# Kernel optimization log

Hardware: AMD Instinct MI355X
Metric: run time of the kernel (lower is better)

## Reference

```python
import jax, jax.numpy as jnp
import numpy as np


def setup_inputs() -> dict:
    key = jax.random.key(0)
    ks = jax.random.split(key, 5)
    B, in_ch, H, W = 8, 256, 128, 128
    C = in_ch // 4
    x = jax.random.normal(ks[0], (B, in_ch, H, W), dtype=jnp.float32)
    # 1x1 conv weights stored as [out_ch, in_ch] (kernel spatial dims are 1)
    w_in = jax.random.normal(ks[1], (C, in_ch), dtype=jnp.float32) * (1.0 / np.sqrt(in_ch))
    b_in = jax.random.normal(ks[2], (C,), dtype=jnp.float32) * 0.01
    w_out = jax.random.normal(ks[3], (in_ch, C), dtype=jnp.float32) * (1.0 / np.sqrt(C))
    b_out = jax.random.normal(ks[4], (in_ch,), dtype=jnp.float32) * 0.01
    detal = jnp.array([0.1], dtype=jnp.float32)
    return {"x": x, "w_in": w_in, "b_in": b_in, "w_out": w_out, "b_out": b_out, "detal": detal}


def _mda(x, w_in, b_in, w_out, b_out, detal):
    # InConv: 1x1 conv == channel GEMM
    inp = jnp.einsum('bihw,oi->bohw', x, w_in) + b_in[None, :, None, None]
    B, C, H, W = inp.shape

    # ---- W branch ----
    # AdaptiveAvgPool2d((None,1)) -> mean over W; softmax over size-1 axis (== ones, kept for faithfulness)
    f_w = jax.nn.softmax(inp.mean(axis=3, keepdims=True), axis=3)          # [B,C,H,1]
    f_w = jnp.transpose(f_w, (0, 3, 1, 2)).reshape(B, C * H, 1)
    Xw = inp.reshape(B, C * H, W)
    Gw = Xw * f_w                                                          # [B,CH,W]
    Tw = jax.nn.softmax(jnp.einsum('bkw,bkv->bwv', Gw, Gw), axis=1)        # [B,W,W], softmax over rows
    Wo = jnp.einsum('bkw,bwv->bkv', Xw, Tw).reshape(B, C, H, W)

    # ---- H branch ----
    f_h = jax.nn.softmax(jnp.transpose(inp, (0, 1, 3, 2)).mean(axis=3, keepdims=True), axis=3)  # [B,C,W,1]
    f_h = jnp.transpose(f_h, (0, 3, 1, 2)).reshape(B, C * W, 1)
    Xh = inp.reshape(B, C * W, H)  # raw .view as in torch (scrambles H/W axes intentionally)
    Gh = Xh * f_h
    Th = jax.nn.softmax(jnp.einsum('bkh,bkg->bhg', Gh, Gh), axis=1)        # [B,H,H]
    Ho = jnp.einsum('bkh,bhg->bkg', Xh, Th).reshape(B, C, H, W)

    # ---- C branch ----
    perm = jnp.transpose(inp, (0, 2, 3, 1))                                # [B,H,W,C]
    f_c = jax.nn.softmax(perm.mean(axis=3, keepdims=True), axis=3)         # [B,H,W,1]
    f_c = jnp.transpose(f_c, (0, 3, 1, 2)).reshape(B, H * W, 1)
    Xc = perm.reshape(B, H * W, C)
    Gc = f_c * Xc
    Tc = jax.nn.softmax(jnp.einsum('bnc,bnd->bcd', Gc, Gc), axis=1)        # [B,C,C]
    # torch does .view(B,C,H,W) on a [B,H*W,C] tensor: raw reshape, NOT a transpose
    Co = jnp.einsum('bnc,bcd->bnd', Xc, Tc).reshape(B, C, H, W)

    s = detal[0] * (Co + Wo + Ho)
    # OuConv 1x1 + residual
    return jnp.einsum('bchw,oc->bohw', s, w_out) + b_out[None, :, None, None] + x


def reference(x, w_in, b_in, w_out, b_out, detal):
    return _mda(x, w_in, b_in, w_out, b_out, detal)
```

## Files before the change

### kernel.cpp

```cpp
#include <hip/hip_runtime.h>
#include <math.h>

#define NB 8
#define IC 256
#define CC 64
#define HH 128
#define WW 128
#define NN (HH*WW)
#define NKW 64
#define NKC 64

static constexpr size_t SZ_INP  = (size_t)NB * CC * NN;
static constexpr size_t OFF_INP = 0;
static constexpr size_t OFF_S   = OFF_INP + SZ_INP;
static constexpr size_t OFF_PC  = OFF_S + SZ_INP;
static constexpr size_t OFF_TW  = OFF_PC + (size_t)NB * NKC * 4096;
static constexpr size_t OFF_TC  = OFF_TW + (size_t)NB * 16384;
static constexpr size_t OFF_WT  = OFF_TC + (size_t)NB * 4096;
static constexpr size_t OFF_WOT = OFF_WT + 16384;

__global__ __launch_bounds__(256) void k_wt(
    const float* __restrict__ w_in, const float* __restrict__ w_out,
    float* __restrict__ w_in_t, float* __restrict__ w_out_t)
{
    const int idx = blockIdx.x * 256 + threadIdx.x;
    if (idx < 16384) {
        const int o = idx & 63, i = idx >> 6;
        w_in_t[idx] = w_in[o * IC + i];
    } else {
        const int j = idx - 16384;
        const int o = j & 255, c = j >> 8;
        w_out_t[j] = w_out[o * CC + c];
    }
}

__global__ __launch_bounds__(256) void k_inconv(
    const float* __restrict__ x, const float* __restrict__ wt,
    const float* __restrict__ b_in, float* __restrict__ inp)
{
    __shared__ float xs[16 * 260];
    __shared__ float wl[16 * 68];
    const int b  = blockIdx.y;
    const int n0 = blockIdx.x * 256;
    const int t  = threadIdx.x;
    const int og = t >> 5;
    const int ng = t & 31;

    const int sr = t >> 4, sc = (t & 15) * 4;
    const float* xbase = x + ((size_t)b * IC + sr) * NN + n0 + sc;
    const float* wbase = wt + (size_t)sr * 64 + sc;
    float* xdst = xs + sr * 260 + sc;
    float* wdst = wl + sr * 68 + sc;

    float acc[8][8];
#pragma unroll
    for (int p = 0; p < 8; p++)
#pragma unroll
        for (int q = 0; q < 8; q++) acc[p][q] = 0.f;

    for (int i0 = 0; i0 < IC; i0 += 16) {
        __syncthreads();
        {
            const float* xsrc = xbase + (size_t)i0 * NN;
            const float4 a0 = *(const float4*)(xsrc);
            const float4 a1 = *(const float4*)(xsrc + 64);
            const float4 a2 = *(const float4*)(xsrc + 128);
            const float4 a3 = *(const float4*)(xsrc + 192);
            const float4 w0 = *(const float4*)(wbase + (size_t)i0 * 64);
            *(float4*)(xdst)       = a0;
            *(float4*)(xdst + 64)  = a1;
            *(float4*)(xdst + 128) = a2;
            *(float4*)(xdst + 192) = a3;
            *(float4*)(wdst)       = w0;
        }
        __syncthreads();
#pragma unroll 4
        for (int i = 0; i < 16; ++i) {
            const float4 wa = *(const float4*)(wl + i * 68 + og * 8);
            const float4 wb = *(const float4*)(wl + i * 68 + og * 8 + 4);
            const float4 xa = *(const float4*)(xs + i * 260 + ng * 4);
            const float4 xb = *(const float4*)(xs + i * 260 + 128 + ng * 4);
            const float wv[8] = {wa.x, wa.y, wa.z, wa.w, wb.x, wb.y, wb.z, wb.w};
            const float xv[8] = {xa.x, xa.y, xa.z, xa.w, xb.x, xb.y, xb.z, xb.w};
#pragma unroll
            for (int p = 0; p < 8; p++)
#pragma unroll
                for (int q = 0; q < 8; q++) acc[p][q] += wv[p] * xv[q];
        }
    }
#pragma unroll
    for (int p = 0; p < 8; ++p) {
        const int oo = og * 8 + p;
        const float bo = b_in[oo];
        float* base = inp + ((size_t)b * CC + oo) * NN + n0;
        *(float4*)(base + ng * 4) =
            make_float4(acc[p][0] + bo, acc[p][1] + bo, acc[p][2] + bo, acc[p][3] + bo);
        *(float4*)(base + 128 + ng * 4) =
            make_float4(acc[p][4] + bo, acc[p][5] + bo, acc[p][6] + bo, acc[p][7] + bo);
    }
}

__global__ __launch_bounds__(256) void k_gramW(const float* __restrict__ inp, float* __restrict__ pW)
{
    __shared__ float xs[32 * 132];
    const int b = blockIdx.y, kc = blockIdx.x;
    const int t = threadIdx.x, tx = t & 15, ty = t >> 4;
    const float* Xb = inp + (size_t)b * CC * NN;
    const int k0 = kc * ((CC * HH) / NKW);

    float acc[8][8];
#pragma unroll
    for (int i = 0; i < 8; i++)
#pragma unroll
        for (int j = 0; j < 8; j++) acc[i][j] = 0.f;

    for (int kk = k0; kk < k0 + (CC * HH) / NKW; kk += 32) {
        __syncthreads();
        {
            const int r = t >> 3, cq = (t & 7) * 16;
            const float* src = Xb + ((size_t)kk + r) * WW + cq;
            float* dst = xs + r * 132 + cq;
#pragma unroll
            for (int j = 0; j < 4; j++)
                *(float4*)(dst + 4 * j) = *(const float4*)(src + 4 * j);
        }
        __syncthreads();
#pragma unroll 8
        for (int k = 0; k < 32; k++) {
            const float* row = xs + k * 132;
            float4 t0 = *(const float4*)(row + ty * 8);
            float4 t1 = *(const float4*)(row + ty * 8 + 4);
            float4 u0 = *(const float4*)(row + tx * 8);
            float4 u1 = *(const float4*)(row + tx * 8 + 4);
            float av[8] = {t0.x, t0.y, t0.z, t0.w, t1.x, t1.y, t1.z, t1.w};
            float bv[8] = {u0.x, u0.y, u0.z, u0.w, u1.x, u1.y, u1.z, u1.w};
#pragma unroll
            for (int i = 0; i < 8; i++)
#pragma unroll
                for (int j = 0; j < 8; j++) acc[i][j] += av[i] * bv[j];
        }
    }
    float* dst = pW + ((size_t)b * NKW + kc) * 16384;
#pragma unroll
    for (int i = 0; i < 8; i++)
#pragma unroll
        for (int j = 0; j < 8; j += 4) {
            float4 v = make_float4(acc[i][j], acc[i][j + 1], acc[i][j + 2], acc[i][j + 3]);
            *(float4*)(dst + (ty * 8 + i) * 128 + tx * 8 + j) = v;
        }
}

__global__ __launch_bounds__(256) void k_redW(const float* __restrict__ pW, float* __restrict__ Tw)
{
    const int b = blockIdx.y;
    const int idx = blockIdx.x * 256 + threadIdx.x;
    const float* p = pW + (size_t)b * NKW * 16384 + idx;
    float acc = 0.f;
#pragma unroll
    for (int k = 0; k < NKW; k++) acc += p[(size_t)k * 16384];
    Tw[(size_t)b * 16384 + idx] = acc;
}

__global__ __launch_bounds__(1024) void k_softW(float* __restrict__ Tw)
{
    __shared__ float red[32 * 33];
    const int b = blockIdx.x, v0 = blockIdx.y * 32;
    const int t = threadIdx.x;
    const int vc = t & 31, wg = t >> 5;
    float* S = Tw + (size_t)b * 16384 + v0 + vc;

    float v[4];
    float m = -3.4e38f;
#pragma unroll
    for (int j = 0; j < 4; j++) { v[j] = S[(wg * 4 + j) * 128]; m = fmaxf(m, v[j]); }
    red[wg * 33 + vc] = m;
    __syncthreads();
    for (int st = 16; st > 0; st >>= 1) {
        if (wg < st) red[wg * 33 + vc] = fmaxf(red[wg * 33 + vc], red[(wg + st) * 33 + vc]);
        __syncthreads();
    }
    m = red[vc];
    __syncthreads();
    float sum = 0.f;
#pragma unroll
    for (int j = 0; j < 4; j++) { v[j] = __expf(v[j] - m); sum += v[j]; }
    red[wg * 33 + vc] = sum;
    __syncthreads();
    for (int st = 16; st > 0; st >>= 1) {
        if (wg < st) red[wg * 33 + vc] += red[(wg + st) * 33 + vc];
        __syncthreads();
    }
    const float inv = 1.f / red[vc];
#pragma unroll
    for (int j = 0; j < 4; j++) S[(wg * 4 + j) * 128] = v[j] * inv;
}

__global__ __launch_bounds__(256) void k_gramC(const float* __restrict__ inp, float* __restrict__ pC)
{
    __shared__ float xt[32 * 68];
    const int b = blockIdx.y, nc = blockIdx.x;
    const int t = threadIdx.x, tx = t & 15, ty = t >> 4;
    const float* ip = inp + (size_t)b * CC * NN;
    const int n0 = nc * (NN / NKC);

    float acc[4][4];
#pragma unroll
    for (int i = 0; i < 4; i++)
#pragma unroll
        for (int j = 0; j < 4; j++) acc[i][j] = 0.f;

    const int scc = t >> 2;
    const int sn  = (t & 3) * 8;

    for (int nt = 0; nt < NN / NKC; nt += 32) {
        __syncthreads();
        {
            const float* src = ip + (size_t)scc * NN + n0 + nt + sn;
            float v[8];
            *(float4*)(v)     = *(const float4*)(src);
            *(float4*)(v + 4) = *(const float4*)(src + 4);
#pragma unroll
            for (int j = 0; j < 8; j++) xt[(sn + j) * 68 + scc] = v[j];
        }
        __syncthreads();
#pragma unroll 8
        for (int nn = 0; nn < 32; nn++) {
            const float4 a4 = *(const float4*)(xt + nn * 68 + ty * 4);
            const float4 e4 = *(const float4*)(xt + nn * 68 + tx * 4);
            const float av[4] = {a4.x, a4.y, a4.z, a4.w};
            const float ev[4] = {e4.x, e4.y, e4.z, e4.w};
#pragma unroll
            for (int i = 0; i < 4; i++)
#pragma unroll
                for (int j = 0; j < 4; j++) acc[i][j] += av[i] * ev[j];
        }
    }
    float* dst = pC + ((size_t)b * NKC + nc) * 4096;
#pragma unroll
    for (int i = 0; i < 4; i++) {
        float4 v = make_float4(acc[i][0], acc[i][1], acc[i][2], acc[i][3]);
        *(float4*)(dst + (ty * 4 + i) * 64 + tx * 4) = v;
    }
}

__global__ __launch_bounds__(256) void k_redC(const float* __restrict__ pC, float* __restrict__ Tc)
{
    const int b = blockIdx.y;
    const int idx = blockIdx.x * 256 + threadIdx.x;
    const float* p = pC + (size_t)b * NKC * 4096 + idx;
    float acc = 0.f;
#pragma unroll
    for (int k = 0; k < NKC; k++) acc += p[(size_t)k * 4096];
    Tc[(size_t)b * 4096 + idx] = acc;
}

__global__ __launch_bounds__(1024) void k_softC(float* __restrict__ Tc)
{
    __shared__ float red[16 * 65];
    const int b = blockIdx.x;
    const int t = threadIdx.x;
    const int dc = t & 63, cg = t >> 6;
    float* S = Tc + (size_t)b * 4096 + dc;

    float v[4];
    float m = -3.4e38f;
#pragma unroll
    for (int j = 0; j < 4; j++) { v[j] = S[(cg * 4 + j) * 64]; m = fmaxf(m, v[j]); }
    red[cg * 65 + dc] = m;
    __syncthreads();
    for (int st = 8; st > 0; st >>= 1) {
        if (cg < st) red[cg * 65 + dc] = fmaxf(red[cg * 65 + dc], red[(cg + st) * 65 + dc]);
        __syncthreads();
    }
    m = red[dc];
    __syncthreads();
    float sum = 0.f;
#pragma unroll
    for (int j = 0; j < 4; j++) { v[j] = __expf(v[j] - m); sum += v[j]; }
    red[cg * 65 + dc] = sum;
    __syncthreads();
    for (int st = 8; st > 0; st >>= 1) {
        if (cg < st) red[cg * 65 + dc] += red[(cg + st) * 65 + dc];
        __syncthreads();
    }
    const float inv = 1.f / red[dc];
#pragma unroll
    for (int j = 0; j < 4; j++) S[(cg * 4 + j) * 64] = v[j] * inv;
}

__global__ __launch_bounds__(256) void k_co(
    const float* __restrict__ inp, const float* __restrict__ Tc,
    const float* __restrict__ detal, float* __restrict__ s)
{
    __shared__ float tc[64 * 68];
    __shared__ float xs[64 * 132];
    const int b  = blockIdx.y;
    const int n0 = blockIdx.x * 128;
    const int t  = threadIdx.x;
    const int d4 = (t & 15) * 4;
    const int g8 = (t >> 4) * 8;

    {
        const int sr = t >> 2, sc = (t & 3) * 4;
        const float* src = inp + ((size_t)b * CC + sr) * NN + n0;
        float* dst = xs + sr * 132;
#pragma unroll
        for (int k = 0; k < 8; k++)
            *(float4*)(dst + sc + 16 * k) = *(const float4*)(src + sc + 16 * k);
        const float* tsrc = Tc + (size_t)b * 4096 + sr * 64;
        float* tdst = tc + sr * 68;
#pragma unroll
        for (int k = 0; k < 4; k++)
            *(float4*)(tdst + sc + 16 * k) = *(const float4*)(tsrc + sc + 16 * k);
    }
    __syncthreads();

    float acc[8][4];
#pragma unroll
    for (int i = 0; i < 8; i++)
#pragma unroll
        for (int j = 0; j < 4; j++) acc[i][j] = 0.f;

#pragma unroll 4
    for (int c = 0; c < 64; c++) {
        const float4 t4 = *(const float4*)(tc + c * 68 + d4);
        const float4 xa = *(const float4*)(xs + c * 132 + g8);
        const float4 xb = *(const float4*)(xs + c * 132 + g8 + 4);
        const float xv[8] = {xa.x, xa.y, xa.z, xa.w, xb.x, xb.y, xb.z, xb.w};
        const float tv[4] = {t4.x, t4.y, t4.z, t4.w};
#pragma unroll
        for (int i = 0; i < 8; i++)
#pragma unroll
            for (int j = 0; j < 4; j++) acc[i][j] += xv[i] * tv[j];
    }
    const float scl = detal[0];
    float* sb = s + (size_t)b * CC * NN + (size_t)n0 * 64;
#pragma unroll
    for (int i = 0; i < 8; i++) {
        float4 v = make_float4(acc[i][0] * scl, acc[i][1] * scl,
                               acc[i][2] * scl, acc[i][3] * scl);
        *(float4*)(sb + (size_t)(g8 + i) * 64 + d4) = v;
    }
}

__global__ __launch_bounds__(128) void k_wo(
    const float* __restrict__ inp, const float* __restrict__ Tw,
    const float* __restrict__ detal, float* __restrict__ s)
{
    __shared__ float xt[32 * 68];
    __shared__ float twl[32 * 132];
    const int b = blockIdx.z, hc = blockIdx.y, c = blockIdx.x;
    const int t = threadIdx.x;
    const int rg = t >> 4;
    const int vg = t & 15;
    const int h0 = hc * 64;

    const float* ip = inp + ((size_t)b * CC + c) * NN + (size_t)h0 * WW;
    const float* twg = Tw + (size_t)b * 16384;

    float acc[8][8];
#pragma unroll
    for (int p = 0; p < 8; p++)
#pragma unroll
        for (int q = 0; q < 8; q++) acc[p][q] = 0.f;

    for (int w0 = 0; w0 < 128; w0 += 32) {
        __syncthreads();
        {
            const int h = t >> 1, wq = (t & 1) * 16;
            const float* src = ip + (size_t)h * WW + w0 + wq;
            float v[16];
            *(float4*)(v)      = *(const float4*)(src);
            *(float4*)(v + 4)  = *(const float4*)(src + 4);
            *(float4*)(v + 8)  = *(const float4*)(src + 8);
            *(float4*)(v + 12) = *(const float4*)(src + 12);
#pragma unroll
            for (int j = 0; j < 16; j++) xt[(wq + j) * 68 + h] = v[j];
        }
        {
            const int w = t >> 2, cq = (t & 3) * 32;
            const float* src = twg + (size_t)(w0 + w) * 128 + cq;
            float* dst = twl + w * 132 + cq;
#pragma unroll
            for (int k = 0; k < 8; k++)
                *(float4*)(dst + 4 * k) = *(const float4*)(src + 4 * k);
        }
        __syncthreads();
#pragma unroll 4
        for (int w = 0; w < 32; ++w) {
            const float4 ra = *(const float4*)(xt + w * 68 + rg * 8);
            const float4 rb = *(const float4*)(xt + w * 68 + rg * 8 + 4);
            const float4 ta = *(const float4*)(twl + w * 132 + vg * 4);
            const float4 tb = *(const float4*)(twl + w * 132 + 64 + vg * 4);
            const float rv[8] = {ra.x, ra.y, ra.z, ra.w, rb.x, rb.y, rb.z, rb.w};
            const float tv[8] = {ta.x, ta.y, ta.z, ta.w, tb.x, tb.y, tb.z, tb.w};
#pragma unroll
            for (int p = 0; p < 8; p++)
#pragma unroll
                for (int q = 0; q < 8; q++) acc[p][q] += rv[p] * tv[q];
        }
    }

    const float sc2 = 2.0f * detal[0];
    float* sp = s + ((size_t)b * CC + c) * NN + (size_t)h0 * WW;
#pragma unroll
    for (int p = 0; p < 8; ++p) {
        const int h = rg * 8 + p;
        float* q0 = sp + (size_t)h * WW + vg * 4;
        float* q1 = sp + (size_t)h * WW + 64 + vg * 4;
        float4 c0 = *(const float4*)q0;
        float4 c1 = *(const float4*)q1;
        c0.x += sc2 * acc[p][0]; c0.y += sc2 * acc[p][1];
        c0.z += sc2 * acc[p][2]; c0.w += sc2 * acc[p][3];
        c1.x += sc2 * acc[p][4]; c1.y += sc2 * acc[p][5];
        c1.z += sc2 * acc[p][6]; c1.w += sc2 * acc[p][7];
        *(float4*)q0 = c0;
        *(float4*)q1 = c1;
    }
}

__global__ __launch_bounds__(256) void k_outconv(
    const float* __restrict__ s, const float* __restrict__ wot,
    const float* __restrict__ b_out, const float* __restrict__ x,
    float* __restrict__ outp)
{
    __shared__ float ss[16 * 68];
    __shared__ float wl[16 * 260];
    const int b  = blockIdx.y;
    const int n0 = blockIdx.x * 64;
    const int t  = threadIdx.x;
    const int og = t >> 3;
    const int ng = t & 7;

    const int sr = t >> 4;
    const int sq = (t & 15) * 4;
    const int wq = (t & 15) * 16;
    const float* sbase = s + ((size_t)b * CC + sr) * NN + n0 + sq;
    const float* wbase = wot + (size_t)sr * IC + wq;
    float* sdst = ss + sr * 68 + sq;
    float* wdst = wl + sr * 260 + wq;

    float acc[8][8];
#pragma unroll
    for (int p = 0; p < 8; p++)
#pragma unroll
        for (int q = 0; q < 8; q++) acc[p][q] = 0.f;

    for (int c0 = 0; c0 < CC; c0 += 16) {
        __syncthreads();
        {
            const float4 a0 = *(const float4*)(sbase + (size_t)c0 * NN);
            const float* wsrc = wbase + (size_t)c0 * IC;
            const float4 w0 = *(const float4*)(wsrc);
            const float4 w1 = *(const float4*)(wsrc + 4);
            const float4 w2 = *(const float4*)(wsrc + 8);
            const float4 w3 = *(const float4*)(wsrc + 12);
            *(float4*)(sdst)      = a0;
            *(float4*)(wdst)      = w0;
            *(float4*)(wdst + 4)  = w1;
            *(float4*)(wdst + 8)  = w2;
            *(float4*)(wdst + 12) = w3;
        }
        __syncthreads();
#pragma unroll 4
        for (int c = 0; c < 16; ++c) {
            const float4 wa = *(const float4*)(wl + c * 260 + og * 8);
            const float4 wb = *(const float4*)(wl + c * 260 + og * 8 + 4);
            const float4 sa = *(const float4*)(ss + c * 68 + ng * 4);
            const float4 sb = *(const float4*)(ss + c * 68 + 32 + ng * 4);
            const float wv[8] = {wa.x, wa.y, wa.z, wa.w, wb.x, wb.y, wb.z, wb.w};
            const float sv[8] = {sa.x, sa.y, sa.z, sa.w, sb.x, sb.y, sb.z, sb.w};
#pragma unroll
            for (int p = 0; p < 8; p++)
#pragma unroll
                for (int q = 0; q < 8; q++) acc[p][q] += wv[p] * sv[q];
        }
    }

#pragma unroll
    for (int p = 0; p < 8; ++p) {
        const int oo = og * 8 + p;
        const float bo = b_out[oo];
        const float* xb = x + ((size_t)b * IC + oo) * NN + n0;
        float* ob = outp + ((size_t)b * IC + oo) * NN + n0;
        const float4 x0 = *(const float4*)(xb + ng * 4);
        const float4 x1 = *(const float4*)(xb + 32 + ng * 4);
        *(float4*)(ob + ng * 4) =
            make_float4(acc[p][0] + bo + x0.x, acc[p][1] + bo + x0.y,
                        acc[p][2] + bo + x0.z, acc[p][3] + bo + x0.w);
        *(float4*)(ob + 32 + ng * 4) =
            make_float4(acc[p][4] + bo + x1.x, acc[p][5] + bo + x1.y,
                        acc[p][6] + bo + x1.z, acc[p][7] + bo + x1.w);
    }
}

extern "C" void kernel_launch(void* const* d_in, const int* in_sizes, int n_in,
                              void* d_out, int out_size, void* d_ws, size_t ws_size,
                              hipStream_t stream)
{
    const float* x     = (const float*)d_in[0];
    const float* w_in  = (const float*)d_in[1];
    const float* b_in  = (const float*)d_in[2];
    const float* w_out = (const float*)d_in[3];
    const float* b_out = (const float*)d_in[4];
    const float* detal = (const float*)d_in[5];
    float* out = (float*)d_out;

    float* ws   = (float*)d_ws;
    float* inp  = ws + OFF_INP;
    float* s    = ws + OFF_S;
    float* pW   = ws + OFF_S;
    float* pC   = ws + OFF_PC;
    float* Tw   = ws + OFF_TW;
    float* Tc   = ws + OFF_TC;
    float* wt   = ws + OFF_WT;
    float* wot  = ws + OFF_WOT;

    k_wt     <<<dim3(128),              256, 0, stream>>>(w_in, w_out, wt, wot);
    k_inconv <<<dim3(NN / 256, NB),     256, 0, stream>>>(x, wt, b_in, inp);
    k_gramW  <<<dim3(NKW, NB),          256, 0, stream>>>(inp, pW);
    k_redW   <<<dim3(64, NB),           256, 0, stream>>>(pW, Tw);
    k_softW  <<<dim3(NB, 4),           1024, 0, stream>>>(Tw);
    k_gramC  <<<dim3(NKC, NB),          256, 0, stream>>>(inp, pC);
    k_redC   <<<dim3(16, NB),           256, 0, stream>>>(pC, Tc);
    k_softC  <<<dim3(NB),              1024, 0, stream>>>(Tc);
    k_co     <<<dim3(NN / 128, NB),     256, 0, stream>>>(inp, Tc, detal, s);
    k_wo     <<<dim3(CC, 2, NB),        128, 0, stream>>>(inp, Tw, detal, s);
    k_outconv<<<dim3(NN / 64, NB),      256, 0, stream>>>(s, wot, b_out, x, out);
}
```

Before: 444.4 us.

## Use fp16 MFMA for input and output 1x1 convolutions

```diff
diff --git a/kernel.cpp b/kernel.cpp
--- a/kernel.cpp
+++ b/kernel.cpp
@@ -10,6 +10,9 @@
 #define NKW 64
 #define NKC 64
 
+typedef _Float16 f16x8 __attribute__((ext_vector_type(8)));
+typedef float f32x4 __attribute__((ext_vector_type(4)));
+
 static constexpr size_t SZ_INP  = (size_t)NB * CC * NN;
 static constexpr size_t OFF_INP = 0;
 static constexpr size_t OFF_S   = OFF_INP + SZ_INP;
@@ -21,83 +24,88 @@
 
 __global__ __launch_bounds__(256) void k_wt(
     const float* __restrict__ w_in, const float* __restrict__ w_out,
-    float* __restrict__ w_in_t, float* __restrict__ w_out_t)
+    _Float16* __restrict__ wh, _Float16* __restrict__ woh)
 {
     const int idx = blockIdx.x * 256 + threadIdx.x;
-    if (idx < 16384) {
-        const int o = idx & 63, i = idx >> 6;
-        w_in_t[idx] = w_in[o * IC + i];
-    } else {
-        const int j = idx - 16384;
-        const int o = j & 255, c = j >> 8;
-        w_out_t[j] = w_out[o * CC + c];
-    }
+    if (idx < 16384) wh[idx] = (_Float16)w_in[idx];
+    else             woh[idx - 16384] = (_Float16)w_out[idx - 16384];
 }
 
 __global__ __launch_bounds__(256) void k_inconv(
-    const float* __restrict__ x, const float* __restrict__ wt,
+    const float* __restrict__ x, const _Float16* __restrict__ wh,
     const float* __restrict__ b_in, float* __restrict__ inp)
 {
-    __shared__ float xs[16 * 260];
-    __shared__ float wl[16 * 68];
+    __shared__ _Float16 wl[64 * 264];
+    __shared__ _Float16 xh[32 * 136];
     const int b  = blockIdx.y;
-    const int n0 = blockIdx.x * 256;
+    const int n0 = blockIdx.x * 128;
     const int t  = threadIdx.x;
-    const int og = t >> 5;
-    const int ng = t & 31;
-
-    const int sr = t >> 4, sc = (t & 15) * 4;
-    const float* xbase = x + ((size_t)b * IC + sr) * NN + n0 + sc;
-    const float* wbase = wt + (size_t)sr * 64 + sc;
-    float* xdst = xs + sr * 260 + sc;
-    float* wdst = wl + sr * 68 + sc;
-
-    float acc[8][8];
-#pragma unroll
-    for (int p = 0; p < 8; p++)
-#pragma unroll
-        for (int q = 0; q < 8; q++) acc[p][q] = 0.f;
-
-    for (int i0 = 0; i0 < IC; i0 += 16) {
+    const int l  = t & 63, wv = t >> 6;
+    const int lr = l & 15, kg = (l >> 4) * 8;
+
+    {
+        const int r = t >> 2, c = (t & 3) * 64;
+        const uint4* src = (const uint4*)(wh + r * 256 + c);
+        uint4* dst = (uint4*)(wl + r * 264 + c);
+#pragma unroll
+        for (int k = 0; k < 8; k++) dst[k] = src[k];
+    }
+
+    f32x4 acc[4][2];
+#pragma unroll
+    for (int mt = 0; mt < 4; mt++)
+#pragma unroll
+        for (int nt = 0; nt < 2; nt++) acc[mt][nt] = (f32x4){0.f, 0.f, 0.f, 0.f};
+
+    for (int kc = 0; kc < 8; ++kc) {
         __syncthreads();
         {
-            const float* xsrc = xbase + (size_t)i0 * NN;
-            const float4 a0 = *(const float4*)(xsrc);
-            const float4 a1 = *(const float4*)(xsrc + 64);
-            const float4 a2 = *(const float4*)(xsrc + 128);
-            const float4 a3 = *(const float4*)(xsrc + 192);
-            const float4 w0 = *(const float4*)(wbase + (size_t)i0 * 64);
-            *(float4*)(xdst)       = a0;
-            *(float4*)(xdst + 64)  = a1;
-            *(float4*)(xdst + 128) = a2;
-            *(float4*)(xdst + 192) = a3;
-            *(float4*)(wdst)       = w0;
-        }
-        __syncthreads();
-#pragma unroll 4
-        for (int i = 0; i < 16; ++i) {
-            const float4 wa = *(const float4*)(wl + i * 68 + og * 8);
-            const float4 wb = *(const float4*)(wl + i * 68 + og * 8 + 4);
-            const float4 xa = *(const float4*)(xs + i * 260 + ng * 4);
-            const float4 xb = *(const float4*)(xs + i * 260 + 128 + ng * 4);
-            const float wv[8] = {wa.x, wa.y, wa.z, wa.w, wb.x, wb.y, wb.z, wb.w};
-            const float xv[8] = {xa.x, xa.y, xa.z, xa.w, xb.x, xb.y, xb.z, xb.w};
-#pragma unroll
-            for (int p = 0; p < 8; p++)
-#pragma unroll
-                for (int q = 0; q < 8; q++) acc[p][q] += wv[p] * xv[q];
-        }
-    }
-#pragma unroll
-    for (int p = 0; p < 8; ++p) {
-        const int oo = og * 8 + p;
-        const float bo = b_in[oo];
-        float* base = inp + ((size_t)b * CC + oo) * NN + n0;
-        *(float4*)(base + ng * 4) =
-            make_float4(acc[p][0] + bo, acc[p][1] + bo, acc[p][2] + bo, acc[p][3] + bo);
-        *(float4*)(base + 128 + ng * 4) =
-            make_float4(acc[p][4] + bo, acc[p][5] + bo, acc[p][6] + bo, acc[p][7] + bo);
-    }
+            const int i = t >> 3, nq = (t & 7) * 16;
+            const float* src = x + ((size_t)b * IC + kc * 32 + i) * NN + n0 + nq;
+            const float4 v0 = *(const float4*)(src);
+            const float4 v1 = *(const float4*)(src + 4);
+            const float4 v2 = *(const float4*)(src + 8);
+            const float4 v3 = *(const float4*)(src + 12);
+            f16x8 h0, h1;
+            h0[0] = (_Float16)v0.x; h0[1] = (_Float16)v0.y;
+            h0[2] = (_Float16)v0.z; h0[3] = (_Float16)v0.w;
+            h0[4] = (_Float16)v1.x; h0[5] = (_Float16)v1.y;
+            h0[6] = (_Float16)v1.z; h0[7] = (_Float16)v1.w;
+            h1[0] = (_Float16)v2.x; h1[1] = (_Float16)v2.y;
+            h1[2] = (_Float16)v2.z; h1[3] = (_Float16)v2.w;
+            h1[4] = (_Float16)v3.x; h1[5] = (_Float16)v3.y;
+            h1[6] = (_Float16)v3.z; h1[7] = (_Float16)v3.w;
+            *(f16x8*)(xh + i * 136 + nq)     = h0;
+            *(f16x8*)(xh + i * 136 + nq + 8) = h1;
+        }
+        __syncthreads();
+
+        f16x8 bf[2];
+#pragma unroll
+        for (int nt = 0; nt < 2; ++nt) {
+            const int n = wv * 32 + nt * 16 + lr;
+#pragma unroll
+            for (int j = 0; j < 8; ++j) bf[nt][j] = xh[(kg + j) * 136 + n];
+        }
+#pragma unroll
+        for (int mt = 0; mt < 4; ++mt) {
+            const f16x8 af = *(const f16x8*)(wl + (mt * 16 + lr) * 264 + kc * 32 + kg);
+            acc[mt][0] = __builtin_amdgcn_mfma_f32_16x16x32_f16(af, bf[0], acc[mt][0], 0, 0, 0);
+            acc[mt][1] = __builtin_amdgcn_mfma_f32_16x16x32_f16(af, bf[1], acc[mt][1], 0, 0, 0);
+        }
+    }
+
+#pragma unroll
+    for (int mt = 0; mt < 4; ++mt)
+#pragma unroll
+        for (int nt = 0; nt < 2; ++nt) {
+            const int n = n0 + wv * 32 + nt * 16 + lr;
+#pragma unroll
+            for (int r = 0; r < 4; ++r) {
+                const int o = mt * 16 + (l >> 4) * 4 + r;
+                inp[((size_t)b * CC + o) * NN + n] = (float)acc[mt][nt][r] + b_in[o];
+            }
+        }
 }
 
 __global__ __launch_bounds__(256) void k_gramW(const float* __restrict__ inp, float* __restrict__ pW)
@@ -420,78 +428,79 @@
 }
 
 __global__ __launch_bounds__(256) void k_outconv(
-    const float* __restrict__ s, const float* __restrict__ wot,
+    const float* __restrict__ s, const _Float16* __restrict__ woh,
     const float* __restrict__ b_out, const float* __restrict__ x,
     float* __restrict__ outp)
 {
-    __shared__ float ss[16 * 68];
-    __shared__ float wl[16 * 260];
+    __shared__ _Float16 wo[256 * 72];
+    __shared__ _Float16 sh[32 * 72];
     const int b  = blockIdx.y;
     const int n0 = blockIdx.x * 64;
     const int t  = threadIdx.x;
-    const int og = t >> 3;
-    const int ng = t & 7;
-
-    const int sr = t >> 4;
-    const int sq = (t & 15) * 4;
-    const int wq = (t & 15) * 16;
-    const float* sbase = s + ((size_t)b * CC + sr) * NN + n0 + sq;
-    const float* wbase = wot + (size_t)sr * IC + wq;
-    float* sdst = ss + sr * 68 + sq;
-    float* wdst = wl + sr * 260 + wq;
-
-    float acc[8][8];
-#pragma unroll
-    for (int p = 0; p < 8; p++)
-#pragma unroll
-        for (int q = 0; q < 8; q++) acc[p][q] = 0.f;
-
-    for (int c0 = 0; c0 < CC; c0 += 16) {
+    const int l  = t & 63, wv = t >> 6;
+    const int lr = l & 15, kg = (l >> 4) * 8;
+
+    {
+        const uint4* src = (const uint4*)(woh + t * 64);
+        uint4* dst = (uint4*)(wo + t * 72);
+#pragma unroll
+        for (int k = 0; k < 4; k++) dst[k] = src[k];
+        const uint4* src2 = src + 4;
+        uint4* dst2 = dst + 4;
+#pragma unroll
+        for (int k = 0; k < 4; k++) dst2[k] = src2[k];
+    }
+
+    f32x4 acc[4][4];
+#pragma unroll
+    for (int mt = 0; mt < 4; mt++)
+#pragma unroll
+        for (int nt = 0; nt < 4; nt++) acc[mt][nt] = (f32x4){0.f, 0.f, 0.f, 0.f};
+
+    for (int kc = 0; kc < 2; ++kc) {
         __syncthreads();
         {
-            const float4 a0 = *(const float4*)(sbase + (size_t)c0 * NN);
-            const float* wsrc = wbase + (size_t)c0 * IC;
-            const float4 w0 = *(const float4*)(wsrc);
-            const float4 w1 = *(const float4*)(wsrc + 4);
-            const float4 w2 = *(const float4*)(wsrc + 8);
-            const float4 w3 = *(const float4*)(wsrc + 12);
-            *(float4*)(sdst)      = a0;
-            *(float4*)(wdst)      = w0;
-            *(float4*)(wdst + 4)  = w1;
-            *(float4*)(wdst + 8)  = w2;
-            *(float4*)(wdst + 12) = w3;
-        }
-        __syncthreads();
-#pragma unroll 4
-        for (int c = 0; c < 16; ++c) {
-            const float4 wa = *(const float4*)(wl + c * 260 + og * 8);
-            const float4 wb = *(const float4*)(wl + c * 260 + og * 8 + 4);
-            const float4 sa = *(const float4*)(ss + c * 68 + ng * 4);
-            const float4 sb = *(const float4*)(ss + c * 68 + 32 + ng * 4);
-            const float wv[8] = {wa.x, wa.y, wa.z, wa.w, wb.x, wb.y, wb.z, wb.w};
-            const float sv[8] = {sa.x, sa.y, sa.z, sa.w, sb.x, sb.y, sb.z, sb.w};
-#pragma unroll
-            for (int p = 0; p < 8; p++)
-#pragma unroll
-                for (int q = 0; q < 8; q++) acc[p][q] += wv[p] * sv[q];
-        }
-    }
-
-#pragma unroll
-    for (int p = 0; p < 8; ++p) {
-        const int oo = og * 8 + p;
-        const float bo = b_out[oo];
-        const float* xb = x + ((size_t)b * IC + oo) * NN + n0;
-        float* ob = outp + ((size_t)b * IC + oo) * NN + n0;
-        const float4 x0 = *(const float4*)(xb + ng * 4);
-        const float4 x1 = *(const float4*)(xb + 32 + ng * 4);
-        *(float4*)(ob + ng * 4) =
-            make_float4(acc[p][0] + bo + x0.x, acc[p][1] + bo + x0.y,
-                        acc[p][2] + bo + x0.z, acc[p][3] + bo + x0.w);
-        *(float4*)(ob + 32 + ng * 4) =
-            make_float4(acc[p][4] + bo + x1.x, acc[p][5] + bo + x1.y,
-                        acc[p][6] + bo + x1.z, acc[p][7] + bo + x1.w);
-    }
+            const int c = t >> 3, n8 = (t & 7) * 8;
+            const float* src = s + ((size_t)b * CC + kc * 32 + c) * NN + n0 + n8;
+            const float4 v0 = *(const float4*)(src);
+            const float4 v1 = *(const float4*)(src + 4);
+            f16x8 h;
+            h[0] = (_Float16)v0.x; h[1] = (_Float16)v0.y;
+            h[2] = (_Float16)v0.z; h[3] = (_Float16)v0.w;
+            h[4] = (_Float16)v1.x; h[5] = (_Float16)v1.y;
+            h[6] = (_Float16)v1.z; h[7] = (_Float16)v1.w;
+            *(f16x8*)(sh + c * 72 + n8) = h;
+        }
+        __syncthreads();
+
+        f16x8 bf[4];
+#pragma unroll
+        for (int nt = 0; nt < 4; ++nt) {
+            const int n = nt * 16 + lr;
+#pragma unroll
+            for (int j = 0; j < 8; ++j) bf[nt][j] = sh[(kg + j) * 72 + n];
+        }
+#pragma unroll
+        for (int mt = 0; mt < 4; ++mt) {
+            const f16x8 af = *(const f16x8*)(wo + (wv * 64 + mt * 16 + lr) * 72 + kc * 32 + kg);
+#pragma unroll
+            for (int nt = 0; nt < 4; ++nt)
+                acc[mt][nt] = __builtin_amdgcn_mfma_f32_16x16x32_f16(af, bf[nt], acc[mt][nt], 0, 0, 0);
+        }
+    }
+
+#pragma unroll
+    for (int mt = 0; mt < 4; ++mt)
+#pragma unroll
+        for (int nt = 0; nt < 4; ++nt) {
+            const int n = n0 + nt * 16 + lr;
+#pragma unroll
+            for (int r = 0; r < 4; ++r) {
+                const int o = wv * 64 + mt * 16 + (l >> 4) * 4 + r;
+                const size_t off = ((size_t)b * IC + o) * NN + n;
+                outp[off] = (float)acc[mt][nt][r] + b_out[o] + x[off];
+            }
+        }
 }
 
 extern "C" void kernel_launch(void* const* d_in, const int* in_sizes, int n_in,
@@ -513,11 +522,11 @@
     float* pC   = ws + OFF_PC;
     float* Tw   = ws + OFF_TW;
     float* Tc   = ws + OFF_TC;
-    float* wt   = ws + OFF_WT;
-    float* wot  = ws + OFF_WOT;
-
-    k_wt     <<<dim3(128),              256, 0, stream>>>(w_in, w_out, wt, wot);
-    k_inconv <<<dim3(NN / 256, NB),     256, 0, stream>>>(x, wt, b_in, inp);
+    _Float16* wh  = (_Float16*)(ws + OFF_WT);
+    _Float16* woh = (_Float16*)(ws + OFF_WOT);
+
+    k_wt     <<<dim3(128),              256, 0, stream>>>(w_in, w_out, wh, woh);
+    k_inconv <<<dim3(NN / 128, NB),     256, 0, stream>>>(x, wh, b_in, inp);
     k_gramW  <<<dim3(NKW, NB),          256, 0, stream>>>(inp, pW);
     k_redW   <<<dim3(64, NB),           256, 0, stream>>>(pW, Tw);
     k_softW  <<<dim3(NB, 4),           1024, 0, stream>>>(Tw);
@@ -526,5 +535,5 @@
     k_softC  <<<dim3(NB),              1024, 0, stream>>>(Tc);
     k_co     <<<dim3(NN / 128, NB),     256, 0, stream>>>(inp, Tc, detal, s);
     k_wo     <<<dim3(CC, 2, NB),        128, 0, stream>>>(inp, Tw, detal, s);
-    k_outconv<<<dim3(NN / 64, NB),      256, 0, stream>>>(s, wot, b_out, x, out);
-}
+    k_outconv<<<dim3(NN / 64, NB),      256, 0, stream>>>(s, woh, b_out, x, out);
+}
```

Result: no change. 445.2 us (+0.2%).
